# Performance work log

Hardware: AMD Instinct MI355X
Metric: run time of the kernel (lower is better)

Reference implementation:

```python
import jax, jax.numpy as jnp
import numpy as np

B, T, NN, H = 16, 64, 4096, 1024  # batch, seq_len, num_nodes**2, gru hidden


def _gru_layer(x, w_ih, w_hh, b_ih, b_hh):
    """PyTorch-semantics GRU layer, batch_first. x: [B, T, in] -> [B, T, H]."""
    h_dim = w_hh.shape[1]
    # precompute all input-side gate projections in one GEMM: [B, T, 3H]
    gates_x = jnp.einsum('bti,gi->btg', x, w_ih) + b_ih

    def step(h, gx):
        gh = h @ w_hh.T + b_hh                      # [B, 3H]
        xr, xz, xn = jnp.split(gx, 3, axis=-1)
        hr, hz, hn = jnp.split(gh, 3, axis=-1)
        r = jax.nn.sigmoid(xr + hr)
        z = jax.nn.sigmoid(xz + hz)
        n = jnp.tanh(xn + r * hn)
        h_new = (1.0 - z) * n + z * h
        return h_new, h_new

    h0 = jnp.zeros((x.shape[0], h_dim), x.dtype)
    _, ys = jax.lax.scan(step, h0, jnp.swapaxes(gates_x, 0, 1))  # time-major scan
    return jnp.swapaxes(ys, 0, 1)


def setup_inputs() -> dict:
    key = jax.random.key(0)
    ks = jax.random.split(key, 12)
    s_in, s_h = 1.0 / np.sqrt(NN), 1.0 / np.sqrt(H)
    return {
        'x':       jax.random.normal(ks[0], (B, T, NN), jnp.float32),
        'w_ih_l0': jax.random.normal(ks[1], (3 * H, NN), jnp.float32) * s_in,
        'w_hh_l0': jax.random.normal(ks[2], (3 * H, H), jnp.float32) * s_h,
        'b_ih_l0': jax.random.normal(ks[3], (3 * H,), jnp.float32) * s_h,
        'b_hh_l0': jax.random.normal(ks[4], (3 * H,), jnp.float32) * s_h,
        'w_ih_l1': jax.random.normal(ks[5], (3 * H, H), jnp.float32) * s_h,
        'w_hh_l1': jax.random.normal(ks[6], (3 * H, H), jnp.float32) * s_h,
        'b_ih_l1': jax.random.normal(ks[7], (3 * H,), jnp.float32) * s_h,
        'b_hh_l1': jax.random.normal(ks[8], (3 * H,), jnp.float32) * s_h,
        'dec_w':   jax.random.normal(ks[9], (NN, H), jnp.float32) * s_h,
        'dec_b':   jax.random.normal(ks[10], (NN,), jnp.float32) * s_h,
    }


def reference(x, w_ih_l0, w_hh_l0, b_ih_l0, b_hh_l0,
              w_ih_l1, w_hh_l1, b_ih_l1, b_hh_l1, dec_w, dec_b):
    # 2-layer GRU encode (batch_first), no dropout (eval / drop_p=0)
    h1 = _gru_layer(x, w_ih_l0, w_hh_l0, b_ih_l0, b_hh_l0)
    h2 = _gru_layer(h1, w_ih_l1, w_hh_l1, b_ih_l1, b_hh_l1)
    last = h2[:, -1, :]                               # [B, H] last timestep
    # per-sample decoder loop in the original == one batched GEMM here
    pred_graph_adj = last @ dec_w.T + dec_b           # [B, num_nodes**2]
    return pred_graph_adj
```

## Files before the change

kernel.cpp:

```cpp
#include <hip/hip_runtime.h>
#include <math.h>

constexpr int kB = 16;
constexpr int kT = 64;
constexpr int kH = 1024;

typedef short bf16x8 __attribute__((ext_vector_type(8)));
typedef float floatx4 __attribute__((ext_vector_type(4)));

__device__ __forceinline__ unsigned short f2bf_rne(float f) {
    unsigned u = __float_as_uint(f);
    u = u + 0x7FFFu + ((u >> 16) & 1u);
    return (unsigned short)(u >> 16);
}
__device__ __forceinline__ unsigned f2bf_fast_u(float f) {
    return (__float_as_uint(f) + 0x8000u) >> 16;
}

__device__ __forceinline__ void store_short_sys(unsigned short* p, unsigned v) {
    asm volatile("global_store_short %0, %1, off sc0 sc1"
                 :: "v"(p), "v"(v) : "memory");
}
__device__ __forceinline__ void store_dword_sys(unsigned* p, unsigned v) {
    asm volatile("global_store_dword %0, %1, off sc0 sc1"
                 :: "v"(p), "v"(v) : "memory");
}
__device__ __forceinline__ unsigned load_dword_sys(const unsigned* p) {
    unsigned v;
    asm volatile("global_load_dword %0, %1, off sc0 sc1\n\t"
                 "s_waitcnt vmcnt(0)"
                 : "=v"(v) : "v"(p) : "memory");
    return v;
}
__device__ __forceinline__ void load3_float_sys(const float* p0, const float* p1,
                                                const float* p2,
                                                float& a, float& b, float& c) {
    asm volatile("global_load_dword %0, %3, off sc0 sc1\n\t"
                 "global_load_dword %1, %4, off sc0 sc1\n\t"
                 "global_load_dword %2, %5, off sc0 sc1\n\t"
                 "s_waitcnt vmcnt(0)"
                 : "=&v"(a), "=&v"(b), "=&v"(c)
                 : "v"(p0), "v"(p1), "v"(p2) : "memory");
}

__device__ __forceinline__ void gload_lds16(const unsigned short* g,
                                            unsigned short* lds) {
    __builtin_amdgcn_global_load_lds(
        (const __attribute__((address_space(1))) unsigned int*)(g),
        (__attribute__((address_space(3))) unsigned int*)(lds), 16, 0, 0);
}

__global__ __launch_bounds__(256)
void pack_bf16_multi(const float* __restrict__ s0, unsigned short* __restrict__ d0, int n0,
                     const float* __restrict__ s1, unsigned short* __restrict__ d1, int n1,
                     const float* __restrict__ s2, unsigned short* __restrict__ d2, int n2,
                     const float* __restrict__ s3, unsigned short* __restrict__ d3, int n3,
                     const float* __restrict__ s4, unsigned short* __restrict__ d4, int n4)
{
    int i = blockIdx.x * 256 + threadIdx.x;
    const float* s; unsigned short* d;
    if (i < n0) { s = s0; d = d0; }
    else { i -= n0;
    if (i < n1) { s = s1; d = d1; }
    else { i -= n1;
    if (i < n2) { s = s2; d = d2; }
    else { i -= n2;
    if (i < n3) { s = s3; d = d3; }
    else { i -= n3;
    if (i >= n4) return; s = s4; d = d4; }}}}
    const float4 v = ((const float4*)s)[i];
    ushort4 o;
    o.x = f2bf_rne(v.x); o.y = f2bf_rne(v.y);
    o.z = f2bf_rne(v.z); o.w = f2bf_rne(v.w);
    ((ushort4*)d)[i] = o;
}

#define GBM 64
#define GBN 64
#define GBK 16
#define GPAD 4

__global__ __launch_bounds__(256)
void gemm_nt_bias(const float* __restrict__ X, const float* __restrict__ W,
                  const float* __restrict__ bias, float* __restrict__ C,
                  int M, int N, int K)
{
    __shared__ float Xs[GBK][GBM + GPAD];
    __shared__ float Ws[GBK][GBN + GPAD];

    const int tid = threadIdx.x;
    const int bm = blockIdx.y * GBM;
    const int bn = blockIdx.x * GBN;
    const int tm = (tid >> 4) * 4;
    const int tn = (tid & 15) * 4;
    const int lr = tid >> 2;
    const int lc = (tid & 3) * 4;

    float acc[4][4] = {};

    for (int k0 = 0; k0 < K; k0 += GBK) {
        {
            const int gr = bm + lr;
            float4 v = make_float4(0.f, 0.f, 0.f, 0.f);
            if (gr < M) v = *(const float4*)(X + (long)gr * K + k0 + lc);
            Xs[lc + 0][lr] = v.x; Xs[lc + 1][lr] = v.y;
            Xs[lc + 2][lr] = v.z; Xs[lc + 3][lr] = v.w;
        }
        {
            const int gr = bn + lr;
            const float4 v = *(const float4*)(W + (long)gr * K + k0 + lc);
            Ws[lc + 0][lr] = v.x; Ws[lc + 1][lr] = v.y;
            Ws[lc + 2][lr] = v.z; Ws[lc + 3][lr] = v.w;
        }
        __syncthreads();
        #pragma unroll
        for (int k = 0; k < GBK; ++k) {
            const float4 a4 = *(const float4*)&Xs[k][tm];
            const float4 b4 = *(const float4*)&Ws[k][tn];
            acc[0][0] += a4.x * b4.x; acc[0][1] += a4.x * b4.y; acc[0][2] += a4.x * b4.z; acc[0][3] += a4.x * b4.w;
            acc[1][0] += a4.y * b4.x; acc[1][1] += a4.y * b4.y; acc[1][2] += a4.y * b4.z; acc[1][3] += a4.y * b4.w;
            acc[2][0] += a4.z * b4.x; acc[2][1] += a4.z * b4.y; acc[2][2] += a4.z * b4.z; acc[2][3] += a4.z * b4.w;
            acc[3][0] += a4.w * b4.x; acc[3][1] += a4.w * b4.y; acc[3][2] += a4.w * b4.z; acc[3][3] += a4.w * b4.w;
        }
        __syncthreads();
    }

    #pragma unroll
    for (int i = 0; i < 4; ++i) {
        const int gr = bm + tm + i;
        if (gr >= M) continue;
        #pragma unroll
        for (int jj = 0; jj < 4; ++jj) {
            const int gc = bn + tn + jj;
            C[(long)gr * N + gc] = acc[i][jj] + bias[gc];
        }
    }
}

#define FLAG_STRIDE 4

__global__ __launch_bounds__(768, 3)
void fused_mega(const unsigned short* __restrict__ xbf,
                const unsigned short* __restrict__ wihbf,
                const float* __restrict__ bih0,
                float* __restrict__ gx0,
                const unsigned short* __restrict__ w0, const float* __restrict__ bb0,
                const unsigned short* __restrict__ w1, const float* __restrict__ bb1,
                const unsigned short* __restrict__ w2, const float* __restrict__ bb2,
                unsigned short* __restrict__ h1bf0, unsigned short* __restrict__ h1bf1,
                unsigned short* __restrict__ h2bf0, unsigned short* __restrict__ h2bf1,
                float* __restrict__ h2last, unsigned* __restrict__ flags)
{
    __shared__ __attribute__((aligned(16))) char smem[49152];

    const int tid = threadIdx.x;
    const int bx  = blockIdx.x;
    const int lane = tid & 63;
    const int wid  = tid >> 6;
    unsigned* const gxflags = flags + 256;

    if (bx >= 64) {
        unsigned short (*As)[2048] = (unsigned short(*)[2048])smem;
        unsigned short (*Bs)[4096] = (unsigned short(*)[4096])(smem + 16384);
        const int widx = bx - 64;
        const int srow = lane >> 2;
        const int scol = (lane & 3) * 8;
        const int al = lane & 15;
        const int aq = lane >> 4;
        const int wm = wid & 1;
        const int wn = wid >> 1;

        for (int pass = 0; pass < 2; ++pass) {
            const int T = widx + pass * 192;
            const int c = T / 24;
            const int n = T % 24;
            const int bn = n * 128;

            const unsigned short* gsrc;
            int ldsoff;
            bool isA;
            if (wid < 4) {
                const int tr = wid * 16 + srow;
                const long grow = (long)((tr >> 2) * 64 + c * 4 + (tr & 3));
                gsrc = xbf + grow * 4096 + scol;
                ldsoff = wid * 512;
                isA = true;
            } else {
                gsrc = wihbf + (long)(bn + (wid - 4) * 16 + srow) * 4096 + scol;
                ldsoff = (wid - 4) * 512;
                isA = false;
            }

            floatx4 acc[2][2];
            #pragma unroll
            for (int i = 0; i < 2; ++i)
                #pragma unroll
                for (int j = 0; j < 2; ++j)
                    acc[i][j] = (floatx4){0.f, 0.f, 0.f, 0.f};

            if (isA) { gload_lds16(gsrc + 0,  &As[0][ldsoff]);
                       gload_lds16(gsrc + 32, &As[1][ldsoff]); }
            else     { gload_lds16(gsrc + 0,  &Bs[0][ldsoff]);
                       gload_lds16(gsrc + 32, &Bs[1][ldsoff]); }

            for (int t = 0; t < 128; ++t) {
                const int k2 = (t + 2 < 128) ? (t + 2) * 32 : t * 32;
                const int b2 = (t + 2) & 3;
                if (isA) gload_lds16(gsrc + k2, &As[b2][ldsoff]);
                else     gload_lds16(gsrc + k2, &Bs[b2][ldsoff]);

                asm volatile("s_waitcnt vmcnt(2)" ::: "memory");
                __builtin_amdgcn_s_barrier();
                asm volatile("" ::: "memory");

                if (wid < 8) {
                    const int cb = t & 3;
                    bf16x8 af[2], bfr[2];
                    #pragma unroll
                    for (int i = 0; i < 2; ++i)
                        af[i] = *(const bf16x8*)&As[cb][(wm * 32 + i * 16 + al) * 32 + aq * 8];
                    #pragma unroll
                    for (int j = 0; j < 2; ++j)
                        bfr[j] = *(const bf16x8*)&Bs[cb][(wn * 32 + j * 16 + al) * 32 + aq * 8];
                    #pragma unroll
                    for (int i = 0; i < 2; ++i)
                        #pragma unroll
                        for (int j = 0; j < 2; ++j)
                            acc[i][j] = __builtin_amdgcn_mfma_f32_16x16x32_bf16(
                                af[i], bfr[j], acc[i][j], 0, 0, 0);
                }
                asm volatile("" ::: "memory");
                __builtin_amdgcn_s_barrier();
            }

            if (wid < 8) {
                #pragma unroll
                for (int i = 0; i < 2; ++i) {
                    #pragma unroll
                    for (int j = 0; j < 2; ++j) {
                        const int col = bn + wn * 32 + j * 16 + al;
                        const float bv = bih0[col];
                        #pragma unroll
                        for (int r = 0; r < 4; ++r) {
                            const int tr = wm * 32 + i * 16 + aq * 4 + r;
                            const long g = (long)((tr >> 2) * 64 + c * 4 + (tr & 3));
                            store_dword_sys((unsigned*)&gx0[g * 3072 + col],
                                            __float_as_uint(acc[i][j][r] + bv));
                        }
                    }
                }
            }
            asm volatile("s_waitcnt vmcnt(0)" ::: "memory");
            __builtin_amdgcn_s_barrier();
            if (tid == 0) store_dword_sys(&gxflags[c * 24 + n], 1u);
        }
        return;
    }

    floatx4 (*part)[3][64] = (floatx4(*)[3][64])smem;

    const int jbase = bx * 16;
    const int ntile = bx >> 3;

    const int m  = wid >> 2;
    const int kh = wid & 3;
    const int al = lane & 15;
    const int aq = lane >> 4;

    const unsigned short* Wm = (m == 0) ? w0 : (m == 1) ? w1 : w2;
    const long wbase = (long)(jbase + al) * kH + kh * 256 + aq * 8;
    bf16x8 wreg[3][8];
    #pragma unroll
    for (int g = 0; g < 3; ++g)
        #pragma unroll
        for (int s = 0; s < 8; ++s)
            wreg[g][s] = *(const bf16x8*)(Wm + (long)g * kH * kH + wbase + s * 32);

    const int ub  = tid >> 4;
    const int ujj = tid & 15;
    const int ujg = jbase + ujj;
    const float b0r = bb0[ujg], b0z = bb0[kH + ujg], b0n = bb0[2 * kH + ujg];
    const float b1r = bb1[ujg], b1z = bb1[kH + ujg], b1n = bb1[2 * kH + ujg];
    const float b2r = bb2[ujg], b2z = bb2[kH + ujg], b2n = bb2[2 * kH + ujg];

    float h1reg = 0.f;
    float h2reg = 0.f;

    const int aoff = al * kH + kh * 256 + aq * 8;
    const int pl   = (ub >> 2) * 16 + ujj;
    const int pr   = ub & 3;

    float gxr = 0.f, gxz = 0.f, gxn = 0.f;
    int readyChunk = -1;
    if (tid < 256) {
        while (load_dword_sys(&gxflags[0 * 24 + ntile]) == 0) {}
        readyChunk = 0;
        const float* g = gx0 + (long)ub * (kT * 3 * kH);
        load3_float_sys(g + ujg, g + kH + ujg, g + 2 * kH + ujg, gxr, gxz, gxn);
    }

    for (int k = 0; k <= kT; ++k) {
        const unsigned short* h1p = (k & 1) ? h1bf0 : h1bf1;
        unsigned short*       h1o = (k & 1) ? h1bf1 : h1bf0;
        const unsigned short* h2p = (k & 1) ? h2bf1 : h2bf0;
        unsigned short*       h2o = (k & 1) ? h2bf0 : h2bf1;

        const bool azero = (m < 2) ? (k == 0) : (k <= 1);
        const unsigned short* hsrc = (m < 2) ? h1p : h2p;
        bf16x8 a[8];
        if (!azero) {
            #pragma unroll
            for (int s = 0; s < 8; ++s)
                asm volatile("global_load_dwordx4 %0, %1, off sc0 sc1"
                             : "=&v"(a[s]) : "v"(hsrc + aoff + s * 32) : "memory");
            asm volatile("s_waitcnt vmcnt(0)" ::: "memory");
            __builtin_amdgcn_sched_barrier(0);
        } else {
            #pragma unroll
            for (int s = 0; s < 8; ++s)
                a[s] = (bf16x8){0, 0, 0, 0, 0, 0, 0, 0};
        }

        floatx4 acc[3];
        #pragma unroll
        for (int g = 0; g < 3; ++g) acc[g] = (floatx4){0.f, 0.f, 0.f, 0.f};
        #pragma unroll
        for (int s = 0; s < 8; ++s)
            #pragma unroll
            for (int g = 0; g < 3; ++g)
                acc[g] = __builtin_amdgcn_mfma_f32_16x16x32_bf16(
                    a[s], wreg[g][s], acc[g], 0, 0, 0);

        #pragma unroll
        for (int g = 0; g < 3; ++g)
            part[wid][g][lane] = acc[g];
        __syncthreads();

        if (tid < 256) {
            float gh[3][3];
            #pragma unroll
            for (int mm = 0; mm < 3; ++mm)
                #pragma unroll
                for (int g = 0; g < 3; ++g)
                    gh[mm][g] = part[mm * 4 + 0][g][pl][pr] + part[mm * 4 + 1][g][pl][pr]
                              + part[mm * 4 + 2][g][pl][pr] + part[mm * 4 + 3][g][pl][pr];

            if (k < kT) {
                const float hr = gh[0][0] + b0r;
                const float hz = gh[0][1] + b0z;
                const float hn = gh[0][2] + b0n;
                const float r = 1.f / (1.f + __expf(-(gxr + hr)));
                const float z = 1.f / (1.f + __expf(-(gxz + hz)));
                const float n = tanhf(gxn + r * hn);
                const float hnew = (1.f - z) * n + z * h1reg;
                h1reg = hnew;
                store_short_sys(h1o + ub * kH + ujg, f2bf_fast_u(hnew));
            }
            if (k > 0) {
                const float xr = gh[1][0] + b1r;
                const float xz = gh[1][1] + b1z;
                const float xn = gh[1][2] + b1n;
                const float hr = gh[2][0] + b2r;
                const float hz = gh[2][1] + b2z;
                const float hn = gh[2][2] + b2n;
                const float r = 1.f / (1.f + __expf(-(xr + hr)));
                const float z = 1.f / (1.f + __expf(-(xz + hz)));
                const float n = tanhf(xn + r * hn);
                const float hnew = (1.f - z) * n + z * h2reg;
                h2reg = hnew;
                store_short_sys(h2o + ub * kH + ujg, f2bf_fast_u(hnew));
                if (k == kT) h2last[(long)ub * kH + ujg] = hnew;
            }
        }

        float nxr = 0.f, nxz = 0.f, nxn = 0.f;
        if (tid < 256 && (k + 1) < kT) {
            const int c2 = (k + 1) >> 2;
            if (c2 != readyChunk) {
                while (load_dword_sys(&gxflags[c2 * 24 + ntile]) == 0) {}
                readyChunk = c2;
            }
            const float* g = gx0 + (long)ub * (kT * 3 * kH) + (long)(k + 1) * 3 * kH;
            load3_float_sys(g + ujg, g + kH + ujg, g + 2 * kH + ujg, nxr, nxz, nxn);
        }

        if (k < kT) {
            __syncthreads();
            if (wid == 0) {
                const unsigned gen = (unsigned)(k + 1);
                if (lane == 0)
                    store_dword_sys(&flags[bx * FLAG_STRIDE], gen);
                while (load_dword_sys(&flags[lane * FLAG_STRIDE]) < gen) {}
            }
            __syncthreads();
        }

        gxr = nxr; gxz = nxz; gxn = nxn;
    }
}

extern "C" void kernel_launch(void* const* d_in, const int* in_sizes, int n_in,
                              void* d_out, int out_size, void* d_ws, size_t ws_size,
                              hipStream_t stream)
{
    const float* x        = (const float*)d_in[0];
    const float* w_ih_l0  = (const float*)d_in[1];
    const float* w_hh_l0  = (const float*)d_in[2];
    const float* b_ih_l0  = (const float*)d_in[3];
    const float* b_hh_l0  = (const float*)d_in[4];
    const float* w_ih_l1  = (const float*)d_in[5];
    const float* w_hh_l1  = (const float*)d_in[6];
    const float* b_ih_l1  = (const float*)d_in[7];
    const float* b_hh_l1  = (const float*)d_in[8];
    const float* dec_w    = (const float*)d_in[9];
    const float* dec_b    = (const float*)d_in[10];
    float* out = (float*)d_out;

    float* ws    = (float*)d_ws;
    float* gx0   = ws;
    unsigned short* h1bf0 = (unsigned short*)(gx0 + (size_t)1024 * 3072);
    unsigned short* h1bf1 = h1bf0 + (size_t)kB * kH;
    unsigned short* h2bf0 = h1bf1 + (size_t)kB * kH;
    unsigned short* h2bf1 = h2bf0 + (size_t)kB * kH;
    float* h2last = (float*)(h2bf1 + (size_t)kB * kH);
    unsigned short* wbf0 = (unsigned short*)(h2last + (size_t)kB * kH);
    unsigned short* wbf1 = wbf0 + (size_t)3 * kH * kH;
    unsigned short* wbf2 = wbf1 + (size_t)3 * kH * kH;
    unsigned short* xbf  = wbf2 + (size_t)3 * kH * kH;
    unsigned short* wihbf = xbf + (size_t)1024 * 4096;
    unsigned* flags = (unsigned*)(wihbf + (size_t)3072 * 4096);

    (void)hipMemsetAsync(flags, 0, 4096, stream);

    const int wn4 = 3 * kH * kH / 4;
    const int xn4 = 1024 * 4096 / 4;
    const int win4 = 3072 * 4096 / 4;
    const int total4 = wn4 * 3 + xn4 + win4;

    pack_bf16_multi<<<(total4 + 255) / 256, 256, 0, stream>>>(
        w_hh_l0, wbf0, wn4,  w_ih_l1, wbf1, wn4,  w_hh_l1, wbf2, wn4,
        x, xbf, xn4,  w_ih_l0, wihbf, win4);

    fused_mega<<<256, 768, 0, stream>>>(
        xbf, wihbf, b_ih_l0, gx0,
        wbf0, b_hh_l0, wbf1, b_ih_l1, wbf2, b_hh_l1,
        h1bf0, h1bf1, h2bf0, h2bf1, h2last, flags);

    gemm_nt_bias<<<dim3(4096 / GBN, 1), 256, 0, stream>>>(
        h2last, dec_w, dec_b, out, kB, 4096, 1024);
}
```

Measured before the change: 629.4 us.

## Replace global grid barrier with per-element tagged hidden-state polling

Each hidden-state element is now stored as a 32-bit word carrying the bf16 value in its upper half and a timestep tag in its lower half. Consumers poll their own input slice until every tag matches the expected step, which removes the all-block flag barrier at each timestep. The trade-off is twice the bytes per hidden-state load, extra repacking work, and a timeout fallback that could read stale data. Launch bounds also drop from 3 to 2 waves per EU, and the tag buffers are zeroed with a memset before launch.

```diff
diff --git a/kernel.cpp b/kernel.cpp
--- a/kernel.cpp
+++ b/kernel.cpp
@@ -7,6 +7,7 @@
 
 typedef short bf16x8 __attribute__((ext_vector_type(8)));
 typedef float floatx4 __attribute__((ext_vector_type(4)));
+typedef unsigned uintx4 __attribute__((ext_vector_type(4)));
 
 __device__ __forceinline__ unsigned short f2bf_rne(float f) {
     unsigned u = __float_as_uint(f);
@@ -17,10 +18,6 @@
     return (__float_as_uint(f) + 0x8000u) >> 16;
 }
 
-__device__ __forceinline__ void store_short_sys(unsigned short* p, unsigned v) {
-    asm volatile("global_store_short %0, %1, off sc0 sc1"
-                 :: "v"(p), "v"(v) : "memory");
-}
 __device__ __forceinline__ void store_dword_sys(unsigned* p, unsigned v) {
     asm volatile("global_store_dword %0, %1, off sc0 sc1"
                  :: "v"(p), "v"(v) : "memory");
@@ -30,6 +27,12 @@
     asm volatile("global_load_dword %0, %1, off sc0 sc1\n\t"
                  "s_waitcnt vmcnt(0)"
                  : "=v"(v) : "v"(p) : "memory");
+    return v;
+}
+__device__ __forceinline__ uintx4 load_x4_sys(const unsigned* p) {
+    uintx4 v;
+    asm volatile("global_load_dwordx4 %0, %1, off sc0 sc1"
+                 : "=&v"(v) : "v"(p) : "memory");
     return v;
 }
 __device__ __forceinline__ void load3_float_sys(const float* p0, const float* p1,
@@ -137,9 +140,9 @@
     }
 }
 
-#define FLAG_STRIDE 4
-
-__global__ __launch_bounds__(768, 3)
+#define POLL_TIMEOUT 20000000LL
+
+__global__ __launch_bounds__(768, 2)
 void fused_mega(const unsigned short* __restrict__ xbf,
                 const unsigned short* __restrict__ wihbf,
                 const float* __restrict__ bih0,
@@ -147,8 +150,8 @@
                 const unsigned short* __restrict__ w0, const float* __restrict__ bb0,
                 const unsigned short* __restrict__ w1, const float* __restrict__ bb1,
                 const unsigned short* __restrict__ w2, const float* __restrict__ bb2,
-                unsigned short* __restrict__ h1bf0, unsigned short* __restrict__ h1bf1,
-                unsigned short* __restrict__ h2bf0, unsigned short* __restrict__ h2bf1,
+                unsigned* __restrict__ h1t0, unsigned* __restrict__ h1t1,
+                unsigned* __restrict__ h2t0, unsigned* __restrict__ h2t1,
                 float* __restrict__ h2last, unsigned* __restrict__ flags)
 {
     __shared__ __attribute__((aligned(16))) char smem[49152];
@@ -286,7 +289,7 @@
     float h1reg = 0.f;
     float h2reg = 0.f;
 
-    const int aoff = al * kH + kh * 256 + aq * 8;
+    const unsigned aoff = al * kH + kh * 256 + aq * 8;
     const int pl   = (ub >> 2) * 16 + ujj;
     const int pr   = ub & 3;
 
@@ -300,21 +303,48 @@
     }
 
     for (int k = 0; k <= kT; ++k) {
-        const unsigned short* h1p = (k & 1) ? h1bf0 : h1bf1;
-        unsigned short*       h1o = (k & 1) ? h1bf1 : h1bf0;
-        const unsigned short* h2p = (k & 1) ? h2bf1 : h2bf0;
-        unsigned short*       h2o = (k & 1) ? h2bf0 : h2bf1;
+        const unsigned* h1p = (k & 1) ? h1t0 : h1t1;
+        unsigned*       h1o = (k & 1) ? h1t1 : h1t0;
+        const unsigned* h2p = (k & 1) ? h2t1 : h2t0;
+        unsigned*       h2o = (k & 1) ? h2t0 : h2t1;
 
         const bool azero = (m < 2) ? (k == 0) : (k <= 1);
-        const unsigned short* hsrc = (m < 2) ? h1p : h2p;
+        const unsigned* hsrc = ((m < 2) ? h1p : h2p) + aoff;
         bf16x8 a[8];
         if (!azero) {
+            const unsigned expg = (unsigned)k;
+            uintx4 t0[8], t1[8];
+            const long long tstart = clock64();
+            for (;;) {
+                #pragma unroll
+                for (int s = 0; s < 8; ++s) {
+                    t0[s] = load_x4_sys(hsrc + s * 32);
+                    t1[s] = load_x4_sys(hsrc + s * 32 + 4);
+                }
+                asm volatile("s_waitcnt vmcnt(0)" ::: "memory");
+                __builtin_amdgcn_sched_barrier(0);
+                bool ok = true;
+                #pragma unroll
+                for (int s = 0; s < 8; ++s) {
+                    ok &= ((t0[s].x & 0xFFFFu) == expg) & ((t0[s].y & 0xFFFFu) == expg)
+                        & ((t0[s].z & 0xFFFFu) == expg) & ((t0[s].w & 0xFFFFu) == expg);
+                    ok &= ((t1[s].x & 0xFFFFu) == expg) & ((t1[s].y & 0xFFFFu) == expg)
+                        & ((t1[s].z & 0xFFFFu) == expg) & ((t1[s].w & 0xFFFFu) == expg);
+                }
+                if (__all(ok)) break;
+                if (clock64() - tstart > POLL_TIMEOUT) break;
+            }
             #pragma unroll
-            for (int s = 0; s < 8; ++s)
-                asm volatile("global_load_dwordx4 %0, %1, off sc0 sc1"
-                             : "=&v"(a[s]) : "v"(hsrc + aoff + s * 32) : "memory");
-            asm volatile("s_waitcnt vmcnt(0)" ::: "memory");
-            __builtin_amdgcn_sched_barrier(0);
+            for (int s = 0; s < 8; ++s) {
+                a[s][0] = (short)(t0[s].x >> 16);
+                a[s][1] = (short)(t0[s].y >> 16);
+                a[s][2] = (short)(t0[s].z >> 16);
+                a[s][3] = (short)(t0[s].w >> 16);
+                a[s][4] = (short)(t1[s].x >> 16);
+                a[s][5] = (short)(t1[s].y >> 16);
+                a[s][6] = (short)(t1[s].z >> 16);
+                a[s][7] = (short)(t1[s].w >> 16);
+            }
         } else {
             #pragma unroll
             for (int s = 0; s < 8; ++s)
@@ -345,6 +375,7 @@
                     gh[mm][g] = part[mm * 4 + 0][g][pl][pr] + part[mm * 4 + 1][g][pl][pr]
                               + part[mm * 4 + 2][g][pl][pr] + part[mm * 4 + 3][g][pl][pr];
 
+            const unsigned wtag = (unsigned)(k + 1);
             if (k < kT) {
                 const float hr = gh[0][0] + b0r;
                 const float hz = gh[0][1] + b0z;
@@ -354,7 +385,8 @@
                 const float n = tanhf(gxn + r * hn);
                 const float hnew = (1.f - z) * n + z * h1reg;
                 h1reg = hnew;
-                store_short_sys(h1o + ub * kH + ujg, f2bf_fast_u(hnew));
+                store_dword_sys(h1o + ub * kH + ujg,
+                                (f2bf_fast_u(hnew) << 16) | wtag);
             }
             if (k > 0) {
                 const float xr = gh[1][0] + b1r;
@@ -368,7 +400,8 @@
                 const float n = tanhf(xn + r * hn);
                 const float hnew = (1.f - z) * n + z * h2reg;
                 h2reg = hnew;
-                store_short_sys(h2o + ub * kH + ujg, f2bf_fast_u(hnew));
+                store_dword_sys(h2o + ub * kH + ujg,
+                                (f2bf_fast_u(hnew) << 16) | wtag);
                 if (k == kT) h2last[(long)ub * kH + ujg] = hnew;
             }
         }
@@ -384,16 +417,7 @@
             load3_float_sys(g + ujg, g + kH + ujg, g + 2 * kH + ujg, nxr, nxz, nxn);
         }
 
-        if (k < kT) {
-            __syncthreads();
-            if (wid == 0) {
-                const unsigned gen = (unsigned)(k + 1);
-                if (lane == 0)
-                    store_dword_sys(&flags[bx * FLAG_STRIDE], gen);
-                while (load_dword_sys(&flags[lane * FLAG_STRIDE]) < gen) {}
-            }
-            __syncthreads();
-        }
+        __syncthreads();
 
         gxr = nxr; gxz = nxz; gxn = nxn;
     }
@@ -418,11 +442,11 @@
 
     float* ws    = (float*)d_ws;
     float* gx0   = ws;
-    unsigned short* h1bf0 = (unsigned short*)(gx0 + (size_t)1024 * 3072);
-    unsigned short* h1bf1 = h1bf0 + (size_t)kB * kH;
-    unsigned short* h2bf0 = h1bf1 + (size_t)kB * kH;
-    unsigned short* h2bf1 = h2bf0 + (size_t)kB * kH;
-    float* h2last = (float*)(h2bf1 + (size_t)kB * kH);
+    unsigned* h1t0 = (unsigned*)(gx0 + (size_t)1024 * 3072);
+    unsigned* h1t1 = h1t0 + (size_t)kB * kH;
+    unsigned* h2t0 = h1t1 + (size_t)kB * kH;
+    unsigned* h2t1 = h2t0 + (size_t)kB * kH;
+    float* h2last = (float*)(h2t1 + (size_t)kB * kH);
     unsigned short* wbf0 = (unsigned short*)(h2last + (size_t)kB * kH);
     unsigned short* wbf1 = wbf0 + (size_t)3 * kH * kH;
     unsigned short* wbf2 = wbf1 + (size_t)3 * kH * kH;
@@ -430,6 +454,7 @@
     unsigned short* wihbf = xbf + (size_t)1024 * 4096;
     unsigned* flags = (unsigned*)(wihbf + (size_t)3072 * 4096);
 
+    (void)hipMemsetAsync(h1t0, 0, 4 * (size_t)kB * kH * sizeof(unsigned), stream);
     (void)hipMemsetAsync(flags, 0, 4096, stream);
 
     const int wn4 = 3 * kH * kH / 4;
@@ -444,7 +469,7 @@
     fused_mega<<<256, 768, 0, stream>>>(
         xbf, wihbf, b_ih_l0, gx0,
         wbf0, b_hh_l0, wbf1, b_ih_l1, wbf2, b_hh_l1,
-        h1bf0, h1bf1, h2bf0, h2bf1, h2last, flags);
+        h1t0, h1t1, h2t0, h2t1, h2last, flags);
 
     gemm_nt_bias<<<dim3(4096 / GBN, 1), 256, 0, stream>>>(
         h2last, dec_w, dec_b, out, kB, 4096, 1024);
```

Measured after the change: 998.0 us. 58.6% more time.
